# Optimization experiments

Measured on AMD Instinct MI355X. Metric: run time of the kernel, lower is better.

## Reference

```python
import jax, jax.numpy as jnp
import numpy as np

B, N, M = 16, 8192, 128  # batch, timesteps, hidden_dim
DT = 1.0


def setup_inputs() -> dict:
    key = jax.random.key(0)
    ks = jax.random.split(key, 12)
    s = 1.0 / np.sqrt(M)
    u = jax.random.normal(ks[0], (B, N, M), dtype=jnp.float32)
    A_diag = jnp.abs(jax.random.normal(ks[1], (M,), dtype=jnp.float32))  # A_max=1.0
    B_w = jax.random.uniform(ks[2], (M, M), jnp.float32, -s, s)
    B_b = jax.random.uniform(ks[3], (M,), jnp.float32, -s, s)
    C_w = jax.random.uniform(ks[4], (M, M), jnp.float32, -s, s)
    C_b = jax.random.uniform(ks[5], (M,), jnp.float32, -s, s)
    D_w = jax.random.uniform(ks[6], (M, M), jnp.float32, -s, s)
    D_b = jax.random.uniform(ks[7], (M,), jnp.float32, -s, s)
    W1 = jax.random.uniform(ks[8], (M, M), jnp.float32, -s, s)
    b1 = jax.random.uniform(ks[9], (M,), jnp.float32, -s, s)
    W2 = jax.random.uniform(ks[10], (M, M), jnp.float32, -s, s)
    b2 = jax.random.uniform(ks[11], (M,), jnp.float32, -s, s)
    return dict(u=u, A_diag=A_diag, B_w=B_w, B_b=B_b, C_w=C_w, C_b=C_b,
                D_w=D_w, D_b=D_b, W1=W1, b1=b1, W2=W2, b2=b2)


def _linoss_im(u, A_diag, B_w, B_b, dt):
    # A = relu(diag(A_diag)); S = (I + dt^2 A)^{-1} is diagonal.
    # M_inv = [[S, -dt*S*A], [dt*S, S]] (all blocks diagonal) -> elementwise recurrence.
    a = jax.nn.relu(A_diag)                       # (m,)
    sdiag = 1.0 / (1.0 + dt * dt * a)             # (m,)
    fz = dt * (jnp.einsum('bnm,km->bnk', u, B_w) + B_b)  # forcing on z-half; y-half is 0
    c_zz = sdiag
    c_zy = -dt * sdiag * a
    c_yz = dt * sdiag
    c_yy = sdiag

    def step(carry, f):
        z, y = carry                              # each (b, m)
        zp = z + f                                # x_{i-1} + F, z-half (y-half forcing is 0)
        z_new = c_zz * zp + c_zy * y
        y_new = c_yz * zp + c_yy * y
        return (z_new, y_new), y_new

    b = u.shape[0]
    m = A_diag.shape[0]
    init = (jnp.zeros((b, m), u.dtype), jnp.zeros((b, m), u.dtype))
    _, ys = jax.lax.scan(step, init, jnp.swapaxes(fz, 0, 1))  # ys: (n, b, m)
    return jnp.swapaxes(ys, 0, 1)                 # (b, n, m) == x[:, :, m:]


def reference(u, A_diag, B_w, B_b, C_w, C_b, D_w, D_b, W1, b1, W2, b2):
    x = _linoss_im(u, A_diag, B_w, B_b, DT)
    # dropout is identity in eval mode
    h = jnp.einsum('bnm,km->bnk', x, C_w) + C_b + jnp.einsum('bnm,km->bnk', u, D_w) + D_b
    h = jax.nn.gelu(h, approximate=False)         # torch GELU default = exact erf
    g = (jnp.einsum('bnm,km->bnk', h, W1) + b1) * jax.nn.sigmoid(
        jnp.einsum('bnm,km->bnk', h, W2) + b2)    # GLU
    return g + u
```

## Files before the change

kernel.cpp:

```cpp
#include <hip/hip_runtime.h>
#include <math.h>

#define Bdim   16
#define Nseq   8192
#define Mdim   128
#define TS     64
#define CHUNKS (Nseq / TS)
#define CHAINS (Bdim * Mdim)
#define NBLK   (Bdim * CHUNKS)

typedef __bf16 bf16;
typedef __bf16 bf16x8 __attribute__((ext_vector_type(8)));
typedef __bf16 bf16x4 __attribute__((ext_vector_type(4)));
typedef float  f32x4  __attribute__((ext_vector_type(4)));

static __device__ __forceinline__ float gelu_exact(float x) {
    return 0.5f * x * (1.0f + erff(x * 0.70710678118654752f));
}

static __device__ __forceinline__ void stage_u(const float* __restrict__ g,
                                               size_t rowBase, bf16* lds, int tid) {
    for (int i = tid; i < TS * 32; i += 256) {
        int r  = i >> 5;
        int c4 = i & 31;
        float4 v = ((const float4*)g)[(rowBase + (size_t)r) * 32 + c4];
        bf16x4 p;
        p[0] = (bf16)v.x; p[1] = (bf16)v.y; p[2] = (bf16)v.z; p[3] = (bf16)v.w;
        *reinterpret_cast<bf16x4*>(&lds[r * 128 + c4 * 4]) = p;
    }
}

static __device__ __forceinline__ void pass_colstrip(const bf16* lA, const bf16* __restrict__ gW,
                                                     f32x4 acc[4][2], int j0, int llo, int lhi) {
    bf16x8 bfr[2][4];
#pragma unroll
    for (int jj = 0; jj < 2; ++jj)
#pragma unroll
        for (int kk = 0; kk < 4; ++kk)
            bfr[jj][kk] = *reinterpret_cast<const bf16x8*>(
                &gW[((j0 + jj) * 16 + llo) * 128 + kk * 32 + lhi * 8]);
#pragma unroll
    for (int kk = 0; kk < 4; ++kk) {
        const int k0 = kk * 32 + lhi * 8;
#pragma unroll
        for (int rt = 0; rt < 4; ++rt) {
            bf16x8 a = *reinterpret_cast<const bf16x8*>(&lA[(rt * 16 + llo) * 128 + k0]);
#pragma unroll
            for (int jj = 0; jj < 2; ++jj)
                acc[rt][jj] = __builtin_amdgcn_mfma_f32_16x16x32_bf16(a, bfr[jj][kk], acc[rt][jj], 0, 0, 0);
        }
    }
}

__global__ __launch_bounds__(256) void kw_conv(const float* __restrict__ Bw,
                                               const float* __restrict__ Cw,
                                               const float* __restrict__ Dw,
                                               const float* __restrict__ W1,
                                               const float* __restrict__ W2,
                                               bf16* __restrict__ wb) {
    const float* s;
    switch (blockIdx.x) {
        case 0:  s = Bw; break;
        case 1:  s = Cw; break;
        case 2:  s = Dw; break;
        case 3:  s = W1; break;
        default: s = W2; break;
    }
    bf16* d = wb + blockIdx.x * 16384;
    for (int i = threadIdx.x; i < 4096; i += 256) {
        float4 v = ((const float4*)s)[i];
        bf16x4 p;
        p[0] = (bf16)v.x; p[1] = (bf16)v.y; p[2] = (bf16)v.z; p[3] = (bf16)v.w;
        ((bf16x4*)d)[i] = p;
    }
}

__global__ __launch_bounds__(256, 4) void kA(const float* __restrict__ u,
                                             const float* __restrict__ Ad,
                                             const float* __restrict__ Bb,
                                             const bf16* __restrict__ Bwb,
                                             float2* __restrict__ stE) {
    __shared__ bf16 buf[TS * 128];
    const int tid  = threadIdx.x;
    const int lane = tid & 63;
    const int wave = tid >> 6;
    const int llo  = lane & 15;
    const int lhi  = lane >> 4;
    const int j0   = wave * 2;
    const size_t rowBase = (size_t)blockIdx.x * TS;

    const int   m   = tid & 127;
    const float a_  = fmaxf(Ad[m], 0.f);
    const float s_  = 1.f / (1.f + a_);
    const float sa_ = s_ * a_;
    float bb[2];
#pragma unroll
    for (int jj = 0; jj < 2; ++jj) bb[jj] = Bb[(j0 + jj) * 16 + llo];

    stage_u(u, rowBase, buf, tid);
    __syncthreads();

    f32x4 acc[4][2];
#pragma unroll
    for (int rt = 0; rt < 4; ++rt)
#pragma unroll
        for (int jj = 0; jj < 2; ++jj) acc[rt][jj] = (f32x4){0.f, 0.f, 0.f, 0.f};
    pass_colstrip(buf, Bwb, acc, j0, llo, lhi);

    __syncthreads();
#pragma unroll
    for (int jj = 0; jj < 2; ++jj) {
        const int col = (j0 + jj) * 16 + llo;
#pragma unroll
        for (int rt = 0; rt < 4; ++rt)
#pragma unroll
            for (int r = 0; r < 4; ++r)
                buf[(rt * 16 + lhi * 4 + r) * 128 + col] = (bf16)(acc[rt][jj][r] + bb[jj]);
    }
    __syncthreads();

    if (tid < 128) {
        float z = 0.f, y = 0.f;
#pragma unroll 8
        for (int t = 0; t < TS; ++t) {
            float f  = (float)buf[t * 128 + m];
            float zp = z + f;
            float yn = s_ * (zp + y);
            z = s_ * zp - sa_ * y;
            y = yn;
        }
        const int b = blockIdx.x >> 7;
        const int c = blockIdx.x & (CHUNKS - 1);
        stE[c * CHAINS + b * Mdim + m] = make_float2(z, y);
    }
}

__global__ __launch_bounds__(64) void kB(const float2* __restrict__ stE,
                                         const float* __restrict__ Ad,
                                         float2* __restrict__ stS) {
    const int chain = blockIdx.x * 64 + threadIdx.x;
    const int m     = chain & 127;
    const float a   = fmaxf(Ad[m], 0.f);
    const float s   = 1.f / (1.f + a);
    float p00 = s, p01 = -s * a, p10 = s, p11 = s;
#pragma unroll
    for (int i = 0; i < 6; ++i) {
        float q00 = p00 * p00 + p01 * p10;
        float q01 = p00 * p01 + p01 * p11;
        float q10 = p10 * p00 + p11 * p10;
        float q11 = p10 * p01 + p11 * p11;
        p00 = q00; p01 = q01; p10 = q10; p11 = q11;
    }
    float tz = 0.f, ty = 0.f;
    for (int c = 0; c < CHUNKS; ++c) {
        stS[c * CHAINS + chain] = make_float2(tz, ty);
        float2 e = stE[c * CHAINS + chain];
        float nz = p00 * tz + p01 * ty + e.x;
        float ny = p10 * tz + p11 * ty + e.y;
        tz = nz; ty = ny;
    }
}

__global__ __launch_bounds__(256, 3) void kC(const float* __restrict__ u,
                                             const float* __restrict__ Ad,
                                             const float* __restrict__ Bb,
                                             const float* __restrict__ Cb,
                                             const float* __restrict__ Db,
                                             const float* __restrict__ b1,
                                             const float* __restrict__ b2,
                                             const bf16* __restrict__ wb,
                                             const float2* __restrict__ stS,
                                             float* __restrict__ out) {
    __shared__ bf16 bufU[TS * 128];
    __shared__ bf16 bufX[TS * 128];
    const bf16* Bwb = wb;
    const bf16* Cwb = wb + 16384;
    const bf16* Dwb = wb + 32768;
    const bf16* W1b = wb + 49152;
    const bf16* W2b = wb + 65536;

    const int tid  = threadIdx.x;
    const int lane = tid & 63;
    const int wave = tid >> 6;
    const int llo  = lane & 15;
    const int lhi  = lane >> 4;
    const int j0   = wave * 2;
    const size_t rowBase = (size_t)blockIdx.x * TS;

    const int   m   = tid & 127;
    const float a_  = fmaxf(Ad[m], 0.f);
    const float s_  = 1.f / (1.f + a_);
    const float sa_ = s_ * a_;
    const int   b   = blockIdx.x >> 7;
    const int   c   = blockIdx.x & (CHUNKS - 1);
    const float2 st = stS[c * CHAINS + b * Mdim + m];
    float bbB[2], bbCD[2], bb1[2], bb2[2];
#pragma unroll
    for (int jj = 0; jj < 2; ++jj) {
        const int col = (j0 + jj) * 16 + llo;
        bbB[jj]  = Bb[col];
        bbCD[jj] = Cb[col] + Db[col];
        bb1[jj]  = b1[col];
        bb2[jj]  = b2[col];
    }

    stage_u(u, rowBase, bufU, tid);
    __syncthreads();

    f32x4 acc[4][2];
#pragma unroll
    for (int rt = 0; rt < 4; ++rt)
#pragma unroll
        for (int jj = 0; jj < 2; ++jj) acc[rt][jj] = (f32x4){0.f, 0.f, 0.f, 0.f};

    pass_colstrip(bufU, Bwb, acc, j0, llo, lhi);
#pragma unroll
    for (int jj = 0; jj < 2; ++jj) {
        const int col = (j0 + jj) * 16 + llo;
#pragma unroll
        for (int rt = 0; rt < 4; ++rt)
#pragma unroll
            for (int r = 0; r < 4; ++r)
                bufX[(rt * 16 + lhi * 4 + r) * 128 + col] = (bf16)(acc[rt][jj][r] + bbB[jj]);
    }
    __syncthreads();

    if (tid < 128) {
        float z = st.x, y = st.y;
#pragma unroll 8
        for (int t = 0; t < TS; ++t) {
            float f  = (float)bufX[t * 128 + m];
            float zp = z + f;
            float yn = s_ * (zp + y);
            z = s_ * zp - sa_ * y;
            y = yn;
            bufX[t * 128 + m] = (bf16)y;
        }
    }
    __syncthreads();

#pragma unroll
    for (int rt = 0; rt < 4; ++rt)
#pragma unroll
        for (int jj = 0; jj < 2; ++jj) acc[rt][jj] = (f32x4){0.f, 0.f, 0.f, 0.f};
    pass_colstrip(bufX, Cwb, acc, j0, llo, lhi);
    pass_colstrip(bufU, Dwb, acc, j0, llo, lhi);
    __syncthreads();
#pragma unroll
    for (int jj = 0; jj < 2; ++jj) {
        const int col = (j0 + jj) * 16 + llo;
#pragma unroll
        for (int rt = 0; rt < 4; ++rt)
#pragma unroll
            for (int r = 0; r < 4; ++r)
                bufX[(rt * 16 + lhi * 4 + r) * 128 + col] =
                    (bf16)gelu_exact(acc[rt][jj][r] + bbCD[jj]);
    }
    __syncthreads();

#pragma unroll
    for (int rt = 0; rt < 4; ++rt)
#pragma unroll
        for (int jj = 0; jj < 2; ++jj) acc[rt][jj] = (f32x4){0.f, 0.f, 0.f, 0.f};
    pass_colstrip(bufX, W2b, acc, j0, llo, lhi);
    f32x4 sig[4][2];
#pragma unroll
    for (int rt = 0; rt < 4; ++rt)
#pragma unroll
        for (int jj = 0; jj < 2; ++jj)
#pragma unroll
            for (int r = 0; r < 4; ++r)
                sig[rt][jj][r] = 1.f / (1.f + expf(-(acc[rt][jj][r] + bb2[jj])));

#pragma unroll
    for (int rt = 0; rt < 4; ++rt)
#pragma unroll
        for (int jj = 0; jj < 2; ++jj) acc[rt][jj] = (f32x4){0.f, 0.f, 0.f, 0.f};
    pass_colstrip(bufX, W1b, acc, j0, llo, lhi);

#pragma unroll
    for (int jj = 0; jj < 2; ++jj) {
        const int col = (j0 + jj) * 16 + llo;
#pragma unroll
        for (int rt = 0; rt < 4; ++rt)
#pragma unroll
            for (int r = 0; r < 4; ++r) {
                const int row = rt * 16 + lhi * 4 + r;
                const size_t idx = (rowBase + row) * 128 + col;
                float g = (acc[rt][jj][r] + bb1[jj]) * sig[rt][jj][r];
                out[idx] = g + u[idx];
            }
    }
}

extern "C" void kernel_launch(void* const* d_in, const int* in_sizes, int n_in,
                              void* d_out, int out_size, void* d_ws, size_t ws_size,
                              hipStream_t stream) {
    const float* u  = (const float*)d_in[0];
    const float* Ad = (const float*)d_in[1];
    const float* Bw = (const float*)d_in[2];
    const float* Bb = (const float*)d_in[3];
    const float* Cw = (const float*)d_in[4];
    const float* Cb = (const float*)d_in[5];
    const float* Dw = (const float*)d_in[6];
    const float* Db = (const float*)d_in[7];
    const float* W1 = (const float*)d_in[8];
    const float* b1 = (const float*)d_in[9];
    const float* W2 = (const float*)d_in[10];
    const float* b2 = (const float*)d_in[11];
    float* out = (float*)d_out;

    char* ws = (char*)d_ws;
    bf16*   wb  = (bf16*)ws;
    float2* stE = (float2*)(ws + 256 * 1024);
    float2* stS = (float2*)(ws + 256 * 1024 + (size_t)CHUNKS * CHAINS * 8);

    kw_conv<<<5, 256, 0, stream>>>(Bw, Cw, Dw, W1, W2, wb);
    kA<<<NBLK, 256, 0, stream>>>(u, Ad, Bb, wb, stE);
    kB<<<CHAINS / 64, 64, 0, stream>>>(stE, Ad, stS);
    kC<<<NBLK, 256, 0, stream>>>(u, Ad, Bb, Cb, Db, b1, b2, wb, stS, out);
}
```

Baseline: 222.8 us.

## Parallelize chunk-state scan with wave shuffles, pad LDS rows, use fast GELU/sigmoid

The serial cross-chunk state propagation kernel becomes a wave-level parallel prefix scan. Each lane handles two chunks and combines partial states with shuffle-up steps, using squared transition matrices. The per-chunk end-state layout changes to chain-major so those loads are contiguous, and LDS rows are padded to 136 elements to reduce bank conflicts in MFMA operand loads. Exact erf GELU and the expf sigmoid are replaced with an Abramowitz–Stegun erfc polynomial and hardware rcp/exp approximations, and kC's occupancy hint rises to 4, at some cost in accuracy.

```diff
diff --git a/kernel.cpp b/kernel.cpp
--- a/kernel.cpp
+++ b/kernel.cpp
@@ -8,14 +8,25 @@
 #define CHUNKS (Nseq / TS)
 #define CHAINS (Bdim * Mdim)
 #define NBLK   (Bdim * CHUNKS)
+#define LDSP   136
 
 typedef __bf16 bf16;
 typedef __bf16 bf16x8 __attribute__((ext_vector_type(8)));
 typedef __bf16 bf16x4 __attribute__((ext_vector_type(4)));
 typedef float  f32x4  __attribute__((ext_vector_type(4)));
 
-static __device__ __forceinline__ float gelu_exact(float x) {
-    return 0.5f * x * (1.0f + erff(x * 0.70710678118654752f));
+static __device__ __forceinline__ float gelu_fast(float x) {
+    float ax = 0.70710678118654752f * fabsf(x);
+    float t  = __builtin_amdgcn_rcpf(fmaf(0.3275911f, ax, 1.0f));
+    float p  = t * fmaf(t, fmaf(t, fmaf(t, fmaf(t, 1.061405429f, -1.453152027f),
+                                        1.421413741f), -0.284496736f), 0.254829592f);
+    float erfc_v = p * __expf(-ax * ax);
+    float half_t = 0.5f * x * erfc_v;
+    return (x >= 0.f) ? x - half_t : half_t;
+}
+
+static __device__ __forceinline__ float sigmoid_fast(float x) {
+    return __builtin_amdgcn_rcpf(1.f + __expf(-x));
 }
 
 static __device__ __forceinline__ void stage_u(const float* __restrict__ g,
@@ -26,7 +37,7 @@
         float4 v = ((const float4*)g)[(rowBase + (size_t)r) * 32 + c4];
         bf16x4 p;
         p[0] = (bf16)v.x; p[1] = (bf16)v.y; p[2] = (bf16)v.z; p[3] = (bf16)v.w;
-        *reinterpret_cast<bf16x4*>(&lds[r * 128 + c4 * 4]) = p;
+        *reinterpret_cast<bf16x4*>(&lds[r * LDSP + c4 * 4]) = p;
     }
 }
 
@@ -44,7 +55,7 @@
         const int k0 = kk * 32 + lhi * 8;
 #pragma unroll
         for (int rt = 0; rt < 4; ++rt) {
-            bf16x8 a = *reinterpret_cast<const bf16x8*>(&lA[(rt * 16 + llo) * 128 + k0]);
+            bf16x8 a = *reinterpret_cast<const bf16x8*>(&lA[(rt * 16 + llo) * LDSP + k0]);
 #pragma unroll
             for (int jj = 0; jj < 2; ++jj)
                 acc[rt][jj] = __builtin_amdgcn_mfma_f32_16x16x32_bf16(a, bfr[jj][kk], acc[rt][jj], 0, 0, 0);
@@ -80,7 +91,7 @@
                                              const float* __restrict__ Bb,
                                              const bf16* __restrict__ Bwb,
                                              float2* __restrict__ stE) {
-    __shared__ bf16 buf[TS * 128];
+    __shared__ bf16 buf[TS * LDSP];
     const int tid  = threadIdx.x;
     const int lane = tid & 63;
     const int wave = tid >> 6;
@@ -115,7 +126,7 @@
         for (int rt = 0; rt < 4; ++rt)
 #pragma unroll
             for (int r = 0; r < 4; ++r)
-                buf[(rt * 16 + lhi * 4 + r) * 128 + col] = (bf16)(acc[rt][jj][r] + bb[jj]);
+                buf[(rt * 16 + lhi * 4 + r) * LDSP + col] = (bf16)(acc[rt][jj][r] + bb[jj]);
     }
     __syncthreads();
 
@@ -123,7 +134,7 @@
         float z = 0.f, y = 0.f;
 #pragma unroll 8
         for (int t = 0; t < TS; ++t) {
-            float f  = (float)buf[t * 128 + m];
+            float f  = (float)buf[t * LDSP + m];
             float zp = z + f;
             float yn = s_ * (zp + y);
             z = s_ * zp - sa_ * y;
@@ -131,14 +142,16 @@
         }
         const int b = blockIdx.x >> 7;
         const int c = blockIdx.x & (CHUNKS - 1);
-        stE[c * CHAINS + b * Mdim + m] = make_float2(z, y);
-    }
-}
-
-__global__ __launch_bounds__(64) void kB(const float2* __restrict__ stE,
-                                         const float* __restrict__ Ad,
-                                         float2* __restrict__ stS) {
-    const int chain = blockIdx.x * 64 + threadIdx.x;
+        stE[(size_t)(b * Mdim + m) * CHUNKS + c] = make_float2(z, y);
+    }
+}
+
+__global__ __launch_bounds__(256) void kB(const float2* __restrict__ stE,
+                                          const float* __restrict__ Ad,
+                                          float2* __restrict__ stS) {
+    const int lane  = threadIdx.x & 63;
+    const int wave  = threadIdx.x >> 6;
+    const int chain = blockIdx.x * 4 + wave;
     const int m     = chain & 127;
     const float a   = fmaxf(Ad[m], 0.f);
     const float s   = 1.f / (1.f + a);
@@ -151,17 +164,38 @@
         float q11 = p10 * p01 + p11 * p11;
         p00 = q00; p01 = q01; p10 = q10; p11 = q11;
     }
-    float tz = 0.f, ty = 0.f;
-    for (int c = 0; c < CHUNKS; ++c) {
-        stS[c * CHAINS + chain] = make_float2(tz, ty);
-        float2 e = stE[c * CHAINS + chain];
-        float nz = p00 * tz + p01 * ty + e.x;
-        float ny = p10 * tz + p11 * ty + e.y;
-        tz = nz; ty = ny;
-    }
-}
-
-__global__ __launch_bounds__(256, 3) void kC(const float* __restrict__ u,
+    const float2 e0 = stE[(size_t)chain * CHUNKS + lane * 2];
+    const float2 e1 = stE[(size_t)chain * CHUNKS + lane * 2 + 1];
+    float vx = p00 * e0.x + p01 * e0.y + e1.x;
+    float vy = p10 * e0.x + p11 * e0.y + e1.y;
+    float q00 = p00 * p00 + p01 * p10;
+    float q01 = p00 * p01 + p01 * p11;
+    float q10 = p10 * p00 + p11 * p10;
+    float q11 = p10 * p01 + p11 * p11;
+#pragma unroll
+    for (int j = 0; j < 6; ++j) {
+        const int d = 1 << j;
+        float ox = __shfl_up(vx, d);
+        float oy = __shfl_up(vy, d);
+        if (lane >= d) {
+            vx = q00 * ox + q01 * oy + vx;
+            vy = q10 * ox + q11 * oy + vy;
+        }
+        float n00 = q00 * q00 + q01 * q10;
+        float n01 = q00 * q01 + q01 * q11;
+        float n10 = q10 * q00 + q11 * q10;
+        float n11 = q10 * q01 + q11 * q11;
+        q00 = n00; q01 = n01; q10 = n10; q11 = n11;
+    }
+    float px = __shfl_up(vx, 1);
+    float py = __shfl_up(vy, 1);
+    if (lane == 0) { px = 0.f; py = 0.f; }
+    stS[(size_t)(2 * lane) * CHAINS + chain] = make_float2(px, py);
+    stS[(size_t)(2 * lane + 1) * CHAINS + chain] =
+        make_float2(p00 * px + p01 * py + e0.x, p10 * px + p11 * py + e0.y);
+}
+
+__global__ __launch_bounds__(256, 4) void kC(const float* __restrict__ u,
                                              const float* __restrict__ Ad,
                                              const float* __restrict__ Bb,
                                              const float* __restrict__ Cb,
@@ -171,8 +205,8 @@
                                              const bf16* __restrict__ wb,
                                              const float2* __restrict__ stS,
                                              float* __restrict__ out) {
-    __shared__ bf16 bufU[TS * 128];
-    __shared__ bf16 bufX[TS * 128];
+    __shared__ bf16 bufU[TS * LDSP];
+    __shared__ bf16 bufX[TS * LDSP];
     const bf16* Bwb = wb;
     const bf16* Cwb = wb + 16384;
     const bf16* Dwb = wb + 32768;
@@ -193,7 +227,7 @@
     const float sa_ = s_ * a_;
     const int   b   = blockIdx.x >> 7;
     const int   c   = blockIdx.x & (CHUNKS - 1);
-    const float2 st = stS[c * CHAINS + b * Mdim + m];
+    const float2 st = stS[(size_t)c * CHAINS + b * Mdim + m];
     float bbB[2], bbCD[2], bb1[2], bb2[2];
 #pragma unroll
     for (int jj = 0; jj < 2; ++jj) {
@@ -221,7 +255,7 @@
         for (int rt = 0; rt < 4; ++rt)
 #pragma unroll
             for (int r = 0; r < 4; ++r)
-                bufX[(rt * 16 + lhi * 4 + r) * 128 + col] = (bf16)(acc[rt][jj][r] + bbB[jj]);
+                bufX[(rt * 16 + lhi * 4 + r) * LDSP + col] = (bf16)(acc[rt][jj][r] + bbB[jj]);
     }
     __syncthreads();
 
@@ -229,12 +263,12 @@
         float z = st.x, y = st.y;
 #pragma unroll 8
         for (int t = 0; t < TS; ++t) {
-            float f  = (float)bufX[t * 128 + m];
+            float f  = (float)bufX[t * LDSP + m];
             float zp = z + f;
             float yn = s_ * (zp + y);
             z = s_ * zp - sa_ * y;
             y = yn;
-            bufX[t * 128 + m] = (bf16)y;
+            bufX[t * LDSP + m] = (bf16)y;
         }
     }
     __syncthreads();
@@ -253,8 +287,8 @@
         for (int rt = 0; rt < 4; ++rt)
 #pragma unroll
             for (int r = 0; r < 4; ++r)
-                bufX[(rt * 16 + lhi * 4 + r) * 128 + col] =
-                    (bf16)gelu_exact(acc[rt][jj][r] + bbCD[jj]);
+                bufX[(rt * 16 + lhi * 4 + r) * LDSP + col] =
+                    (bf16)gelu_fast(acc[rt][jj][r] + bbCD[jj]);
     }
     __syncthreads();
 
@@ -270,7 +304,7 @@
         for (int jj = 0; jj < 2; ++jj)
 #pragma unroll
             for (int r = 0; r < 4; ++r)
-                sig[rt][jj][r] = 1.f / (1.f + expf(-(acc[rt][jj][r] + bb2[jj])));
+                sig[rt][jj][r] = sigmoid_fast(acc[rt][jj][r] + bb2[jj]);
 
 #pragma unroll
     for (int rt = 0; rt < 4; ++rt)
@@ -317,6 +351,6 @@
 
     kw_conv<<<5, 256, 0, stream>>>(Bw, Cw, Dw, W1, W2, wb);
     kA<<<NBLK, 256, 0, stream>>>(u, Ad, Bb, wb, stE);
-    kB<<<CHAINS / 64, 64, 0, stream>>>(stE, Ad, stS);
+    kB<<<CHAINS / 4, 256, 0, stream>>>(stE, Ad, stS);
     kC<<<NBLK, 256, 0, stream>>>(u, Ad, Bb, Cb, Db, b1, b2, wb, stS, out);
 }
```

New measurement: 215.1 us. 1.04x faster.
